# Optimization experiments

Hardware: AMD Instinct MI355X
Metric: run time of the kernel (lower is better)

## Reference

```python
import jax, jax.numpy as jnp
import numpy as np

N_QUBITS = 4

def _rx(theta):
    # RX(t) = [[cos t/2, -i sin t/2], [-i sin t/2, cos t/2]]; theta scalar or [B]
    c = jnp.cos(theta / 2).astype(jnp.complex64)
    s = (-1j * jnp.sin(theta / 2)).astype(jnp.complex64)
    return jnp.stack([jnp.stack([c, s], -1), jnp.stack([s, c], -1)], -2)

def _ry(theta):
    c = jnp.cos(theta / 2).astype(jnp.complex64)
    s = jnp.sin(theta / 2).astype(jnp.complex64)
    return jnp.stack([jnp.stack([c, -s], -1), jnp.stack([s, c], -1)], -2)

def _rz(theta):
    e0 = jnp.exp(-0.5j * theta).astype(jnp.complex64)
    e1 = jnp.exp(0.5j * theta).astype(jnp.complex64)
    z = jnp.zeros_like(e0)
    return jnp.stack([jnp.stack([e0, z], -1), jnp.stack([z, e1], -1)], -2)

def _apply_1q(psi, U, wire):
    # psi: [B,2,2,2,2]; U: [2,2] (shared) or [B,2,2] (per-batch angle)
    psi = jnp.moveaxis(psi, 1 + wire, -1)
    if U.ndim == 3:
        psi = jnp.einsum('bij,b...j->b...i', U, psi)
    else:
        psi = jnp.einsum('ij,b...j->b...i', U, psi)
    return jnp.moveaxis(psi, -1, 1 + wire)

def _cnot(psi, c, t):
    psi = jnp.moveaxis(psi, (1 + c, 1 + t), (-2, -1))
    psi = jnp.concatenate([psi[..., 0:1, :], psi[..., 1:2, ::-1]], axis=-2)
    return jnp.moveaxis(psi, (-2, -1), (1 + c, 1 + t))

def _measure_all_z(psi):
    p = psi.real ** 2 + psi.imag ** 2  # [B,2,2,2,2]
    outs = []
    for w in range(N_QUBITS):
        shape = [1] * (N_QUBITS + 1)
        shape[1 + w] = 2
        z = jnp.array([1.0, -1.0], dtype=p.dtype).reshape(shape)
        outs.append(jnp.sum(p * z, axis=tuple(range(1, N_QUBITS + 1))))
    return jnp.stack(outs, -1)  # [B,4]

def _qlayer(x, theta):
    # x: [B,4] encoding angles; theta: [4] trainable RX angles
    B = x.shape[0]
    psi = jnp.zeros((B, 2 ** N_QUBITS), jnp.complex64).at[:, 0].set(1.0)
    psi = psi.reshape((B,) + (2,) * N_QUBITS)
    # encoder: rx(w0), ry(w1), rz(w2), rx(w3)
    psi = _apply_1q(psi, _rx(x[:, 0]), 0)
    psi = _apply_1q(psi, _ry(x[:, 1]), 1)
    psi = _apply_1q(psi, _rz(x[:, 2]), 2)
    psi = _apply_1q(psi, _rx(x[:, 3]), 3)
    # trainable RX on each wire
    for w in range(N_QUBITS):
        psi = _apply_1q(psi, _rx(theta[w]), w)
    # CNOT ring 0->1,1->2,2->3,3->0
    for w in range(N_QUBITS):
        psi = _cnot(psi, w, (w + 1) % N_QUBITS)
    return _measure_all_z(psi)

def setup_inputs() -> dict:
    key = jax.random.key(0)
    ks = jax.random.split(key, 13)
    T, B, D, H, Q = 128, 2048, 128, 4, 4
    s = 1.0 / np.sqrt(D + H)
    inp = {
        'inputs': jax.random.normal(ks[0], (T, B, D), jnp.float32),
        'Wf': jax.random.uniform(ks[1], (Q, D + H), jnp.float32, -s, s),
        'bf': jax.random.uniform(ks[2], (Q,), jnp.float32, -s, s),
        'Wi': jax.random.uniform(ks[3], (Q, D + H), jnp.float32, -s, s),
        'bi': jax.random.uniform(ks[4], (Q,), jnp.float32, -s, s),
        'Wu': jax.random.uniform(ks[5], (Q, D + H), jnp.float32, -s, s),
        'bu': jax.random.uniform(ks[6], (Q,), jnp.float32, -s, s),
        'Wo': jax.random.uniform(ks[7], (Q, D + H), jnp.float32, -s, s),
        'bo': jax.random.uniform(ks[8], (Q,), jnp.float32, -s, s),
        'theta_f': jax.random.uniform(ks[9], (Q,), jnp.float32, 0.0, 2 * np.pi),
        'theta_i': jax.random.uniform(ks[10], (Q,), jnp.float32, 0.0, 2 * np.pi),
        'theta_u': jax.random.uniform(ks[11], (Q,), jnp.float32, 0.0, 2 * np.pi),
        'theta_o': jax.random.uniform(ks[12], (Q,), jnp.float32, 0.0, 2 * np.pi),
    }
    return inp

def reference(inputs, Wf, bf, Wi, bi, Wu, bu, Wo, bo, theta_f, theta_i, theta_u, theta_o):
    T, B, D = inputs.shape
    H = N_QUBITS  # hidden_dim == n_qubits (required by elementwise gate math)
    h0 = jnp.zeros((B, H), inputs.dtype)
    c0 = jnp.zeros((B, H), inputs.dtype)

    def step(carry, x):
        hx, cx = carry
        comb = jnp.concatenate([x, hx], axis=1)  # [B, D+H]
        f = jax.nn.sigmoid(_qlayer(comb @ Wf.T + bf, theta_f))
        i = jax.nn.sigmoid(_qlayer(comb @ Wi.T + bi, theta_i))
        g = jnp.tanh(_qlayer(comb @ Wu.T + bu, theta_u))
        o = jax.nn.sigmoid(_qlayer(comb @ Wo.T + bo, theta_o))
        cx = f * cx + i * g
        hx = o * jnp.tanh(cx)
        return (hx, cx), hx

    (hx, cx), stacked = jax.lax.scan(step, (h0, c0), inputs)
    return stacked, hx, cx
```

## Files before the change

kernel.cpp:

```cpp
#include <hip/hip_runtime.h>
#include <stdint.h>

__device__ __forceinline__ float fast_exp(float x) {
  return __builtin_amdgcn_exp2f(x * 1.4426950408889634f);
}
__device__ __forceinline__ float fast_rcp(float x) {
  return __builtin_amdgcn_rcpf(x);
}
__device__ __forceinline__ float fast_cos(float x) {
  return __builtin_amdgcn_cosf(__builtin_amdgcn_fractf(x * 0.15915494309189535f));
}
__device__ __forceinline__ float fast_sigmoid(float x) {
  return fast_rcp(1.0f + fast_exp(-x));
}
__device__ __forceinline__ float fast_tanh(float x) {
  return 1.0f - 2.0f * fast_rcp(1.0f + fast_exp(2.0f * x));
}
__device__ __forceinline__ float sigmoid_poly(float x) {
  float x2 = x * x;
  float p = fmaf(fmaf(fmaf(-2.1085373e-4f, x2, 2.0833334e-3f), x2,
                      -2.0833334e-2f), x2, 0.25f);
  return fmaf(x, p, 0.5f);
}
__device__ __forceinline__ float tanh_pade(float x) {
  float x2 = x * x;
  float num = x * fmaf(x2 + 105.f, x2, 945.f);
  float den = fmaf(fmaf(15.f, x2, 420.f), x2, 945.f);
  return num * fast_rcp(den);
}

template <int CTRL>
__device__ __forceinline__ float dppf(float v) {
  return __int_as_float(__builtin_amdgcn_update_dpp(
      0, __float_as_int(v), CTRL, 0xf, 0xf, true));
}
#define QP_XOR1 0xB1
#define QP_XOR2 0x4E
#define QP_XOR3 0x1B

__global__ __launch_bounds__(64) void qlstm_gemm(
    const float* __restrict__ x,
    const float* __restrict__ Wf, const float* __restrict__ bf,
    const float* __restrict__ Wi, const float* __restrict__ bi,
    const float* __restrict__ Wu, const float* __restrict__ bu,
    const float* __restrict__ Wo, const float* __restrict__ bo,
    const float* __restrict__ thf, const float* __restrict__ thi,
    const float* __restrict__ thu, const float* __restrict__ tho,
    float* __restrict__ Z, long long rows, int B, int D)
{
  __shared__ float tile[64][36];
  const long long base = (long long)blockIdx.x * 64;
  const int tid = threadIdx.x;
  const long long r = base + tid;
  const bool valid = r < rows;
  const int ldw = D + 4;
  const float* Ws[4] = {Wf, Wi, Wu, Wo};
  const float* bs[4] = {bf, bi, bu, bo};
  const float* ts[4] = {thf, thi, thu, tho};

  float acc[12];
#pragma unroll
  for (int g = 0; g < 4; ++g) {
    acc[g * 3 + 0] = bs[g][0] + ts[g][0];
    acc[g * 3 + 1] = bs[g][1];
    acc[g * 3 + 2] = bs[g][3] + ts[g][3];
  }

  const int nkc = D >> 5;
  for (int kc = 0; kc < nkc; ++kc) {
#pragma unroll
    for (int i = 0; i < 8; ++i) {
      int f = i * 64 + tid;
      int row = f >> 3, col = (f & 7) * 4;
      long long gr = base + row;
      if (gr < rows) {
        float4 v = *(const float4*)(x + gr * (long long)D + kc * 32 + col);
        *(float4*)&tile[row][col] = v;
      }
    }
    __syncthreads();
    if (valid) {
#pragma unroll
      for (int k = 0; k < 32; k += 4) {
        float4 xv = *(float4*)&tile[tid][k];
#pragma unroll
        for (int g = 0; g < 4; ++g) {
#pragma unroll
          for (int jj = 0; jj < 3; ++jj) {
            int row2 = (jj == 2) ? 3 : jj;
            const float* wp = Ws[g] + row2 * ldw + kc * 32 + k;
            acc[g * 3 + jj] += xv.x * wp[0] + xv.y * wp[1] + xv.z * wp[2] + xv.w * wp[3];
          }
        }
      }
    }
    __syncthreads();
  }

  if (valid) {
    float* zp = Z + r * 16;
#pragma unroll
    for (int g = 0; g < 4; ++g) {
      *(float4*)(zp + g * 4) =
          make_float4(acc[g * 3 + 0], acc[g * 3 + 1], acc[g * 3 + 2], 0.f);
    }
  }
}

__global__ __launch_bounds__(64) void qlstm_scan4(
    const float* __restrict__ Z,
    const float* __restrict__ Wf, const float* __restrict__ Wi,
    const float* __restrict__ Wu, const float* __restrict__ Wo,
    const float* __restrict__ thf, const float* __restrict__ thi,
    const float* __restrict__ thu, const float* __restrict__ tho,
    float* __restrict__ out, int T, int B, int D)
{
  const int gid = blockIdx.x * 64 + threadIdx.x;
  const int b = gid >> 2, q = gid & 3;
  if (b >= B) return;

  const float* Wg = (q == 0) ? Wf : (q == 1) ? Wi : (q == 2) ? Wu : Wo;
  const float* th = (q == 0) ? thf : (q == 1) ? thi : (q == 2) ? thu : tho;
  const int ldw = D + 4;
  const float ct1 = fast_cos(th[1]);
  const float m2c = fast_cos(th[2]);

  float wh[3][4];
#pragma unroll
  for (int jj = 0; jj < 3; ++jj) {
    int row = (jj == 2) ? 3 : jj;
#pragma unroll
    for (int d = 0; d < 4; ++d)
      wh[jj][d] = Wg[row * ldw + D + (q ^ d)];
  }
  const bool e0 = ((q & 1) == 0);
  const bool e1 = ((q & 2) == 0);

  float h = 0.f, c = 0.f;

  const float* Zg = Z + (size_t)gid * 4;
  const size_t tstr = (size_t)16 * B;
  const size_t pstr = (size_t)4 * B;
  float* hx  = out + (size_t)T * B * 4;
  float* cxp = hx + (size_t)B * 4;

  auto ld1 = [&](int t) -> float4 {
    return *(const float4*)(Zg + (size_t)t * tstr);
  };

  auto step = [&](float4 zv, int t) {
    float z0 = zv.x, z1 = zv.y, z2 = zv.z;
    float h1 = dppf<QP_XOR1>(h);
    float h2 = dppf<QP_XOR2>(h);
    float h3 = dppf<QP_XOR3>(h);
    float a0 = fmaf(wh[0][0], h, fmaf(wh[0][1], h1, fmaf(wh[0][2], h2, fmaf(wh[0][3], h3, z0))));
    float a1 = fmaf(wh[1][0], h, fmaf(wh[1][1], h1, fmaf(wh[1][2], h2, fmaf(wh[1][3], h3, z1))));
    float a2 = fmaf(wh[2][0], h, fmaf(wh[2][1], h1, fmaf(wh[2][2], h2, fmaf(wh[2][3], h3, z2))));
    float m0 = fast_cos(a0);
    float m1 = ct1 * fast_cos(a1);
    float m3 = fast_cos(a2);
    float m01 = m0 * m1, m23 = m2c * m3;
    float g0 = m1 * m23;
    float g1 = m01;
    float g2 = m01 * m2c;
    float g3 = m01 * m23;
    float x0 = dppf<QP_XOR1>(g0);
    float x1 = dppf<QP_XOR1>(g1);
    float x2 = dppf<QP_XOR1>(g2);
    float x3 = dppf<QP_XOR1>(g3);
    float s0 = e0 ? g0 : x1;
    float s1 = e0 ? x0 : g1;
    float s2 = e0 ? g2 : x3;
    float s3 = e0 ? x2 : g3;
    float y0 = dppf<QP_XOR2>(s0);
    float y1 = dppf<QP_XOR2>(s1);
    float y2 = dppf<QP_XOR2>(s2);
    float y3 = dppf<QP_XOR2>(s3);
    float wf_ = e1 ? s0 : y2;
    float wi_ = e1 ? s1 : y3;
    float wu_ = e1 ? y0 : s2;
    float wo_ = e1 ? y1 : s3;
    float fg = sigmoid_poly(wf_);
    float ig = sigmoid_poly(wi_);
    float ug = tanh_pade(wu_);
    float og = sigmoid_poly(wo_);
    c = fmaf(fg, c, ig * ug);
    h = og * tanh_pade(c);
    out[(size_t)t * pstr + gid] = h;
  };

  float4 A, Bv, C, Dv, E, F, G, H;
  if (T > 0) A  = ld1(0);
  if (T > 1) Bv = ld1(1);
  if (T > 2) C  = ld1(2);
  if (T > 3) Dv = ld1(3);
  if (T > 4) E  = ld1(4);
  if (T > 5) F  = ld1(5);
  if (T > 6) G  = ld1(6);
  if (T > 7) H  = ld1(7);

  int T8 = T & ~7;
  for (int t = 0; t < T8; t += 8) {
    { float4 zv = A;  if (t + 8  < T) A  = ld1(t + 8);  step(zv, t);     }
    { float4 zv = Bv; if (t + 9  < T) Bv = ld1(t + 9);  step(zv, t + 1); }
    { float4 zv = C;  if (t + 10 < T) C  = ld1(t + 10); step(zv, t + 2); }
    { float4 zv = Dv; if (t + 11 < T) Dv = ld1(t + 11); step(zv, t + 3); }
    { float4 zv = E;  if (t + 12 < T) E  = ld1(t + 12); step(zv, t + 4); }
    { float4 zv = F;  if (t + 13 < T) F  = ld1(t + 13); step(zv, t + 5); }
    { float4 zv = G;  if (t + 14 < T) G  = ld1(t + 14); step(zv, t + 6); }
    { float4 zv = H;  if (t + 15 < T) H  = ld1(t + 15); step(zv, t + 7); }
  }
  for (int t = T8; t < T; ++t) {
    step(ld1(t), t);
  }
  hx[gid]  = h;
  cxp[gid] = c;
}

struct GK {
  float wh[4][3][4];
  float ct1[4];
  float m2c[4];
};

__device__ __forceinline__ void load_gk(GK& K,
    const float* Wf, const float* Wi, const float* Wu, const float* Wo,
    const float* thf, const float* thi, const float* thu, const float* tho,
    int D)
{
  const float* Ws[4] = {Wf, Wi, Wu, Wo};
  const float* ts[4] = {thf, thi, thu, tho};
  const int ldw = D + 4;
#pragma unroll
  for (int g = 0; g < 4; ++g) {
#pragma unroll
    for (int jj = 0; jj < 3; ++jj) {
      int row = (jj == 2) ? 3 : jj;
#pragma unroll
      for (int qq = 0; qq < 4; ++qq)
        K.wh[g][jj][qq] = Ws[g][row * ldw + D + qq];
    }
    K.ct1[g] = fast_cos(ts[g][1]);
    K.m2c[g] = fast_cos(ts[g][2]);
  }
}

__device__ __forceinline__ void qlstm_step_sc(const float a[12], const GK& K,
                                              float h[4], float c[4])
{
  float gv[4][4];
#pragma unroll
  for (int g = 0; g < 4; ++g) {
    float m0 = fast_cos(a[g * 3 + 0]);
    float m1 = K.ct1[g] * fast_cos(a[g * 3 + 1]);
    float m3 = fast_cos(a[g * 3 + 2]);
    float m01 = m0 * m1;
    float m23 = K.m2c[g] * m3;
    gv[g][0] = m1 * m23;
    gv[g][1] = m01;
    gv[g][2] = m01 * K.m2c[g];
    gv[g][3] = m01 * m23;
  }
#pragma unroll
  for (int qq = 0; qq < 4; ++qq) {
    float fg = fast_sigmoid(gv[0][qq]);
    float ig = fast_sigmoid(gv[1][qq]);
    float ug = fast_tanh(gv[2][qq]);
    float og = fast_sigmoid(gv[3][qq]);
    c[qq] = fg * c[qq] + ig * ug;
    h[qq] = og * fast_tanh(c[qq]);
  }
}

__global__ __launch_bounds__(256) void qlstm_fused(
    const float* __restrict__ x,
    const float* __restrict__ Wf, const float* __restrict__ bf,
    const float* __restrict__ Wi, const float* __restrict__ bi,
    const float* __restrict__ Wu, const float* __restrict__ bu,
    const float* __restrict__ Wo, const float* __restrict__ bo,
    const float* __restrict__ thf, const float* __restrict__ thi,
    const float* __restrict__ thu, const float* __restrict__ tho,
    float* __restrict__ out, int T, int B, int D)
{
  int b = blockIdx.x * 256 + threadIdx.x;
  if (b >= B) return;
  GK K;
  load_gk(K, Wf, Wi, Wu, Wo, thf, thi, thu, tho, D);
  const float* Ws[4] = {Wf, Wi, Wu, Wo};
  const float* bs[4] = {bf, bi, bu, bo};
  const float* ts[4] = {thf, thi, thu, tho};
  const int ldw = D + 4;

  float base[12];
#pragma unroll
  for (int g = 0; g < 4; ++g) {
    base[g * 3 + 0] = bs[g][0] + ts[g][0];
    base[g * 3 + 1] = bs[g][1];
    base[g * 3 + 2] = bs[g][3] + ts[g][3];
  }

  float h[4] = {0.f, 0.f, 0.f, 0.f};
  float c[4] = {0.f, 0.f, 0.f, 0.f};
  float* hx  = out + (size_t)T * B * 4;
  float* cxp = hx + (size_t)B * 4;

  for (int t = 0; t < T; ++t) {
    float a[12];
#pragma unroll
    for (int j = 0; j < 12; ++j) a[j] = base[j];
    const float* xp = x + ((size_t)t * B + b) * D;
    for (int k = 0; k < D; k += 4) {
      float4 xv = *(const float4*)(xp + k);
#pragma unroll
      for (int g = 0; g < 4; ++g) {
        const float* W = Ws[g];
#pragma unroll
        for (int jj = 0; jj < 3; ++jj) {
          int row = (jj == 2) ? 3 : jj;
          const float* wp = W + row * ldw + k;
          a[g * 3 + jj] += xv.x * wp[0] + xv.y * wp[1] + xv.z * wp[2] + xv.w * wp[3];
        }
      }
    }
#pragma unroll
    for (int g = 0; g < 4; ++g) {
#pragma unroll
      for (int jj = 0; jj < 3; ++jj) {
        a[g * 3 + jj] += K.wh[g][jj][0] * h[0] + K.wh[g][jj][1] * h[1]
                       + K.wh[g][jj][2] * h[2] + K.wh[g][jj][3] * h[3];
      }
    }
    qlstm_step_sc(a, K, h, c);
    *(float4*)(out + ((size_t)t * B + b) * 4) = make_float4(h[0], h[1], h[2], h[3]);
  }
  *(float4*)(hx + (size_t)b * 4)  = make_float4(h[0], h[1], h[2], h[3]);
  *(float4*)(cxp + (size_t)b * 4) = make_float4(c[0], c[1], c[2], c[3]);
}

extern "C" void kernel_launch(void* const* d_in, const int* in_sizes, int n_in,
                              void* d_out, int out_size, void* d_ws, size_t ws_size,
                              hipStream_t stream)
{
  const float* x   = (const float*)d_in[0];
  const float* Wf  = (const float*)d_in[1];
  const float* bf  = (const float*)d_in[2];
  const float* Wi  = (const float*)d_in[3];
  const float* bi  = (const float*)d_in[4];
  const float* Wu  = (const float*)d_in[5];
  const float* bu  = (const float*)d_in[6];
  const float* Wo  = (const float*)d_in[7];
  const float* bo  = (const float*)d_in[8];
  const float* thf = (const float*)d_in[9];
  const float* thi = (const float*)d_in[10];
  const float* thu = (const float*)d_in[11];
  const float* tho = (const float*)d_in[12];

  int DH = in_sizes[1] / 4;
  int D  = DH - 4;
  long long TB = (long long)in_sizes[0] / D;
  int B = (int)(((long long)out_size - 4 * TB) / 8);
  int T = (int)(TB / B);

  size_t zbytes = (size_t)TB * 16 * sizeof(float);
  if (ws_size >= zbytes && (D & 31) == 0) {
    float* Z = (float*)d_ws;
    int gblocks = (int)((TB + 63) / 64);
    qlstm_gemm<<<gblocks, 64, 0, stream>>>(x, Wf, bf, Wi, bi, Wu, bu, Wo, bo,
                                           thf, thi, thu, tho, Z, TB, B, D);
    int sthreads = B * 4;
    qlstm_scan4<<<(sthreads + 63) / 64, 64, 0, stream>>>(Z, Wf, Wi, Wu, Wo,
                                                         thf, thi, thu, tho,
                                                         (float*)d_out, T, B, D);
  } else {
    qlstm_fused<<<(B + 255) / 256, 256, 0, stream>>>(x, Wf, bf, Wi, bi, Wu, bu, Wo, bo,
                                                     thf, thi, thu, tho,
                                                     (float*)d_out, T, B, D);
  }
}
```

Baseline: 70.50 us.

## Prefetch scan inputs into LDS via async global_load_lds double buffering

```diff
diff --git a/kernel.cpp b/kernel.cpp
--- a/kernel.cpp
+++ b/kernel.cpp
@@ -37,6 +37,15 @@
 #define QP_XOR1 0xB1
 #define QP_XOR2 0x4E
 #define QP_XOR3 0x1B
+
+__device__ __forceinline__ void gload_lds16(const float* gp, const float* lp) {
+  __builtin_amdgcn_global_load_lds(
+      reinterpret_cast<const uint32_t __attribute__((address_space(1)))*>(
+          reinterpret_cast<uintptr_t>(gp)),
+      reinterpret_cast<uint32_t __attribute__((address_space(3)))*>(
+          reinterpret_cast<uintptr_t>(lp)),
+      16, 0, 0);
+}
 
 __global__ __launch_bounds__(64) void qlstm_gemm(
     const float* __restrict__ x,
@@ -115,7 +124,9 @@
     const float* __restrict__ thu, const float* __restrict__ tho,
     float* __restrict__ out, int T, int B, int D)
 {
-  const int gid = blockIdx.x * 64 + threadIdx.x;
+  __shared__ float lds[2][16][256];
+  const int tid = threadIdx.x;
+  const int gid = blockIdx.x * 64 + tid;
   const int b = gid >> 2, q = gid & 3;
   if (b >= B) return;
 
@@ -138,15 +149,11 @@
 
   float h = 0.f, c = 0.f;
 
-  const float* Zg = Z + (size_t)gid * 4;
+  const float* Zlane = Z + (size_t)gid * 4;
   const size_t tstr = (size_t)16 * B;
   const size_t pstr = (size_t)4 * B;
   float* hx  = out + (size_t)T * B * 4;
   float* cxp = hx + (size_t)B * 4;
-
-  auto ld1 = [&](int t) -> float4 {
-    return *(const float4*)(Zg + (size_t)t * tstr);
-  };
 
   auto step = [&](float4 zv, int t) {
     float z0 = zv.x, z1 = zv.y, z2 = zv.z;
@@ -189,30 +196,45 @@
     out[(size_t)t * pstr + gid] = h;
   };
 
-  float4 A, Bv, C, Dv, E, F, G, H;
-  if (T > 0) A  = ld1(0);
-  if (T > 1) Bv = ld1(1);
-  if (T > 2) C  = ld1(2);
-  if (T > 3) Dv = ld1(3);
-  if (T > 4) E  = ld1(4);
-  if (T > 5) F  = ld1(5);
-  if (T > 6) G  = ld1(6);
-  if (T > 7) H  = ld1(7);
-
-  int T8 = T & ~7;
-  for (int t = 0; t < T8; t += 8) {
-    { float4 zv = A;  if (t + 8  < T) A  = ld1(t + 8);  step(zv, t);     }
-    { float4 zv = Bv; if (t + 9  < T) Bv = ld1(t + 9);  step(zv, t + 1); }
-    { float4 zv = C;  if (t + 10 < T) C  = ld1(t + 10); step(zv, t + 2); }
-    { float4 zv = Dv; if (t + 11 < T) Dv = ld1(t + 11); step(zv, t + 3); }
-    { float4 zv = E;  if (t + 12 < T) E  = ld1(t + 12); step(zv, t + 4); }
-    { float4 zv = F;  if (t + 13 < T) F  = ld1(t + 13); step(zv, t + 5); }
-    { float4 zv = G;  if (t + 14 < T) G  = ld1(t + 14); step(zv, t + 6); }
-    { float4 zv = H;  if (t + 15 < T) H  = ld1(t + 15); step(zv, t + 7); }
-  }
-  for (int t = T8; t < T; ++t) {
-    step(ld1(t), t);
-  }
+  auto issue_chunk = [&](int tbase, int buf) {
+#pragma unroll
+    for (int tl = 0; tl < 16; ++tl) {
+      gload_lds16(Zlane + (size_t)(tbase + tl) * tstr, &lds[buf][tl][0]);
+    }
+  };
+
+  if (T >= 32 && (T & 15) == 0) {
+    const int nch = T >> 4;
+    issue_chunk(0, 0);
+    issue_chunk(16, 1);
+    asm volatile("s_waitcnt vmcnt(16)" ::: "memory");
+    __builtin_amdgcn_sched_barrier(0);
+    int cur = 0;
+    for (int k = 0; k < nch; ++k) {
+      const int tb = k << 4;
+#pragma unroll
+      for (int tl = 0; tl < 16; ++tl) {
+        float4 zv = *(const float4*)&lds[cur][tl][tid * 4];
+        step(zv, tb + tl);
+      }
+      if (k + 2 < nch) issue_chunk((k + 2) << 4, cur);
+      cur ^= 1;
+      if (k + 1 < nch) {
+        if (k + 2 < nch) {
+          asm volatile("s_waitcnt vmcnt(32)" ::: "memory");
+        } else {
+          asm volatile("s_waitcnt vmcnt(16)" ::: "memory");
+        }
+        __builtin_amdgcn_sched_barrier(0);
+      }
+    }
+  } else {
+    for (int t = 0; t < T; ++t) {
+      float4 zv = *(const float4*)(Zlane + (size_t)t * tstr);
+      step(zv, t);
+    }
+  }
+
   hx[gid]  = h;
   cxp[gid] = c;
 }
@@ -362,7 +384,7 @@
   int T = (int)(TB / B);
 
   size_t zbytes = (size_t)TB * 16 * sizeof(float);
-  if (ws_size >= zbytes && (D & 31) == 0) {
+  if (ws_size >= zbytes && (D & 31) == 0 && (B & 15) == 0) {
     float* Z = (float*)d_ws;
     int gblocks = (int)((TB + 63) / 64);
     qlstm_gemm<<<gblocks, 64, 0, stream>>>(x, Wf, bf, Wi, bi, Wu, bu, Wo, bo,
```

Measured after the change: 71.61 us. About the same (+1.6%).

## Interleave two independent batch recurrences per thread and prescale cos arguments

Applied to the files above, without the earlier changes.

```diff
diff --git a/kernel.cpp b/kernel.cpp
--- a/kernel.cpp
+++ b/kernel.cpp
@@ -9,6 +9,9 @@
 }
 __device__ __forceinline__ float fast_cos(float x) {
   return __builtin_amdgcn_cosf(__builtin_amdgcn_fractf(x * 0.15915494309189535f));
+}
+__device__ __forceinline__ float cos_rev(float x) {
+  return __builtin_amdgcn_cosf(__builtin_amdgcn_fractf(x));
 }
 __device__ __forceinline__ float fast_sigmoid(float x) {
   return fast_rcp(1.0f + fast_exp(-x));
@@ -37,6 +40,8 @@
 #define QP_XOR1 0xB1
 #define QP_XOR2 0x4E
 #define QP_XOR3 0x1B
+
+#define INV2PI 0.15915494309189535f
 
 __global__ __launch_bounds__(64) void qlstm_gemm(
     const float* __restrict__ x,
@@ -101,13 +106,14 @@
     float* zp = Z + r * 16;
 #pragma unroll
     for (int g = 0; g < 4; ++g) {
-      *(float4*)(zp + g * 4) =
-          make_float4(acc[g * 3 + 0], acc[g * 3 + 1], acc[g * 3 + 2], 0.f);
-    }
-  }
-}
-
-__global__ __launch_bounds__(64) void qlstm_scan4(
+      *(float4*)(zp + g * 4) = make_float4(acc[g * 3 + 0] * INV2PI,
+                                           acc[g * 3 + 1] * INV2PI,
+                                           acc[g * 3 + 2] * INV2PI, 0.f);
+    }
+  }
+}
+
+__global__ __launch_bounds__(64) void qlstm_scan4x2(
     const float* __restrict__ Z,
     const float* __restrict__ Wf, const float* __restrict__ Wi,
     const float* __restrict__ Wu, const float* __restrict__ Wo,
@@ -115,9 +121,11 @@
     const float* __restrict__ thu, const float* __restrict__ tho,
     float* __restrict__ out, int T, int B, int D)
 {
-  const int gid = blockIdx.x * 64 + threadIdx.x;
-  const int b = gid >> 2, q = gid & 3;
-  if (b >= B) return;
+  const int tid = threadIdx.x;
+  const int quad = tid >> 2, q = tid & 3;
+  const int bA = blockIdx.x * 32 + quad;
+  const int bB = bA + 16;
+  if (bB >= B) return;
 
   const float* Wg = (q == 0) ? Wf : (q == 1) ? Wi : (q == 2) ? Wu : Wo;
   const float* th = (q == 0) ? thf : (q == 1) ? thi : (q == 2) ? thu : tho;
@@ -131,24 +139,26 @@
     int row = (jj == 2) ? 3 : jj;
 #pragma unroll
     for (int d = 0; d < 4; ++d)
-      wh[jj][d] = Wg[row * ldw + D + (q ^ d)];
+      wh[jj][d] = Wg[row * ldw + D + (q ^ d)] * INV2PI;
   }
   const bool e0 = ((q & 1) == 0);
   const bool e1 = ((q & 2) == 0);
 
-  float h = 0.f, c = 0.f;
-
-  const float* Zg = Z + (size_t)gid * 4;
+  float hA = 0.f, cA = 0.f, hB = 0.f, cB = 0.f;
+
   const size_t tstr = (size_t)16 * B;
   const size_t pstr = (size_t)4 * B;
+  const size_t slotA = (size_t)(bA * 4 + q);
+  const size_t slotB = (size_t)(bB * 4 + q);
+  const float* ZA = Z + slotA * 4;
+  const float* ZB = Z + slotB * 4;
   float* hx  = out + (size_t)T * B * 4;
   float* cxp = hx + (size_t)B * 4;
 
-  auto ld1 = [&](int t) -> float4 {
-    return *(const float4*)(Zg + (size_t)t * tstr);
-  };
-
-  auto step = [&](float4 zv, int t) {
+  auto ldA = [&](int t) -> float4 { return *(const float4*)(ZA + (size_t)t * tstr); };
+  auto ldB = [&](int t) -> float4 { return *(const float4*)(ZB + (size_t)t * tstr); };
+
+  auto step = [&](float4 zv, float& h, float& c, size_t oidx) {
     float z0 = zv.x, z1 = zv.y, z2 = zv.z;
     float h1 = dppf<QP_XOR1>(h);
     float h2 = dppf<QP_XOR2>(h);
@@ -156,9 +166,9 @@
     float a0 = fmaf(wh[0][0], h, fmaf(wh[0][1], h1, fmaf(wh[0][2], h2, fmaf(wh[0][3], h3, z0))));
     float a1 = fmaf(wh[1][0], h, fmaf(wh[1][1], h1, fmaf(wh[1][2], h2, fmaf(wh[1][3], h3, z1))));
     float a2 = fmaf(wh[2][0], h, fmaf(wh[2][1], h1, fmaf(wh[2][2], h2, fmaf(wh[2][3], h3, z2))));
-    float m0 = fast_cos(a0);
-    float m1 = ct1 * fast_cos(a1);
-    float m3 = fast_cos(a2);
+    float m0 = cos_rev(a0);
+    float m1 = ct1 * cos_rev(a1);
+    float m3 = cos_rev(a2);
     float m01 = m0 * m1, m23 = m2c * m3;
     float g0 = m1 * m23;
     float g1 = m01;
@@ -186,35 +196,42 @@
     float og = sigmoid_poly(wo_);
     c = fmaf(fg, c, ig * ug);
     h = og * tanh_pade(c);
-    out[(size_t)t * pstr + gid] = h;
+    out[oidx] = h;
   };
 
-  float4 A, Bv, C, Dv, E, F, G, H;
-  if (T > 0) A  = ld1(0);
-  if (T > 1) Bv = ld1(1);
-  if (T > 2) C  = ld1(2);
-  if (T > 3) Dv = ld1(3);
-  if (T > 4) E  = ld1(4);
-  if (T > 5) F  = ld1(5);
-  if (T > 6) G  = ld1(6);
-  if (T > 7) H  = ld1(7);
-
-  int T8 = T & ~7;
-  for (int t = 0; t < T8; t += 8) {
-    { float4 zv = A;  if (t + 8  < T) A  = ld1(t + 8);  step(zv, t);     }
-    { float4 zv = Bv; if (t + 9  < T) Bv = ld1(t + 9);  step(zv, t + 1); }
-    { float4 zv = C;  if (t + 10 < T) C  = ld1(t + 10); step(zv, t + 2); }
-    { float4 zv = Dv; if (t + 11 < T) Dv = ld1(t + 11); step(zv, t + 3); }
-    { float4 zv = E;  if (t + 12 < T) E  = ld1(t + 12); step(zv, t + 4); }
-    { float4 zv = F;  if (t + 13 < T) F  = ld1(t + 13); step(zv, t + 5); }
-    { float4 zv = G;  if (t + 14 < T) G  = ld1(t + 14); step(zv, t + 6); }
-    { float4 zv = H;  if (t + 15 < T) H  = ld1(t + 15); step(zv, t + 7); }
-  }
-  for (int t = T8; t < T; ++t) {
-    step(ld1(t), t);
-  }
-  hx[gid]  = h;
-  cxp[gid] = c;
+  float4 A0, A1, A2, A3, Bb0, Bb1, Bb2, Bb3;
+  if (T > 0) { A0 = ldA(0); Bb0 = ldB(0); }
+  if (T > 1) { A1 = ldA(1); Bb1 = ldB(1); }
+  if (T > 2) { A2 = ldA(2); Bb2 = ldB(2); }
+  if (T > 3) { A3 = ldA(3); Bb3 = ldB(3); }
+
+  int T4 = T & ~3;
+  for (int t = 0; t < T4; t += 4) {
+    { float4 za = A0, zb = Bb0;
+      if (t + 4 < T) { A0 = ldA(t + 4); Bb0 = ldB(t + 4); }
+      size_t o = (size_t)t * pstr;
+      step(za, hA, cA, o + slotA); step(zb, hB, cB, o + slotB); }
+    { float4 za = A1, zb = Bb1;
+      if (t + 5 < T) { A1 = ldA(t + 5); Bb1 = ldB(t + 5); }
+      size_t o = (size_t)(t + 1) * pstr;
+      step(za, hA, cA, o + slotA); step(zb, hB, cB, o + slotB); }
+    { float4 za = A2, zb = Bb2;
+      if (t + 6 < T) { A2 = ldA(t + 6); Bb2 = ldB(t + 6); }
+      size_t o = (size_t)(t + 2) * pstr;
+      step(za, hA, cA, o + slotA); step(zb, hB, cB, o + slotB); }
+    { float4 za = A3, zb = Bb3;
+      if (t + 7 < T) { A3 = ldA(t + 7); Bb3 = ldB(t + 7); }
+      size_t o = (size_t)(t + 3) * pstr;
+      step(za, hA, cA, o + slotA); step(zb, hB, cB, o + slotB); }
+  }
+  for (int t = T4; t < T; ++t) {
+    size_t o = (size_t)t * pstr;
+    step(ldA(t), hA, cA, o + slotA);
+    step(ldB(t), hB, cB, o + slotB);
+  }
+
+  hx[slotA]  = hA;  hx[slotB]  = hB;
+  cxp[slotA] = cA;  cxp[slotB] = cB;
 }
 
 struct GK {
@@ -362,15 +379,17 @@
   int T = (int)(TB / B);
 
   size_t zbytes = (size_t)TB * 16 * sizeof(float);
-  if (ws_size >= zbytes && (D & 31) == 0) {
+  bool ok = (ws_size >= zbytes) && ((D & 31) == 0) && ((B & 31) == 0) &&
+            ((TB & 63) == 0);
+  if (ok) {
     float* Z = (float*)d_ws;
-    int gblocks = (int)((TB + 63) / 64);
+    int gblocks = (int)(TB / 64);
     qlstm_gemm<<<gblocks, 64, 0, stream>>>(x, Wf, bf, Wi, bi, Wu, bu, Wo, bo,
                                            thf, thi, thu, tho, Z, TB, B, D);
-    int sthreads = B * 4;
-    qlstm_scan4<<<(sthreads + 63) / 64, 64, 0, stream>>>(Z, Wf, Wi, Wu, Wo,
-                                                         thf, thi, thu, tho,
-                                                         (float*)d_out, T, B, D);
+    int sblocks = B / 32;
+    qlstm_scan4x2<<<sblocks, 64, 0, stream>>>(Z, Wf, Wi, Wu, Wo,
+                                              thf, thi, thu, tho,
+                                              (float*)d_out, T, B, D);
   } else {
     qlstm_fused<<<(B + 255) / 256, 256, 0, stream>>>(x, Wf, bf, Wi, bi, Wu, bu, Wo, bo,
                                                      thf, thi, thu, tho,
```

After: 87.90 us. 1.25x slower.
